# Kernel optimization log

Hardware: AMD Instinct MI355X
Metric: run time of the kernel (lower is better)

## Reference

```python
import jax, jax.numpy as jnp
import numpy as np

SEQ_LEN = 4096
HIDDEN = 1280
NUM_HEADS = 16
HEAD_DIM = HIDDEN // NUM_HEADS  # 80
NUM_SEQS = 8


def setup_inputs() -> dict:
    key = jax.random.key(0)
    ks = jax.random.split(key, 8)
    x = jax.random.normal(ks[0], (SEQ_LEN, HIDDEN), dtype=jnp.float32)
    # rotary tables: use cos/sin of random angles so they are bounded like real RoPE tables
    ang = jax.random.uniform(ks[1], (SEQ_LEN, HEAD_DIM), dtype=jnp.float32) * 6.283185
    cos = jnp.cos(ang)
    sin = jnp.sin(ang)
    # variable-length packed segments: strictly increasing boundaries incl. 0 and SEQ_LEN
    rng = np.random.default_rng(0)
    inner = np.sort(rng.choice(np.arange(1, SEQ_LEN), size=NUM_SEQS - 1, replace=False))
    cu_seqlens = jnp.asarray(np.concatenate([[0], inner, [SEQ_LEN]]), dtype=jnp.int32)
    s = 0.02
    w_qkv = jax.random.normal(ks[2], (HIDDEN, 3 * HIDDEN), dtype=jnp.float32) * s
    b_qkv = jnp.zeros((3 * HIDDEN,), dtype=jnp.float32)
    w_proj = jax.random.normal(ks[3], (HIDDEN, HIDDEN), dtype=jnp.float32) * s
    b_proj = jnp.zeros((HIDDEN,), dtype=jnp.float32)
    return {"x": x, "cu_seqlens": cu_seqlens, "cos": cos, "sin": sin,
            "w_qkv": w_qkv, "b_qkv": b_qkv, "w_proj": w_proj, "b_proj": b_proj}


def _rotate_half(t):
    d = t.shape[-1] // 2
    return jnp.concatenate([-t[..., d:], t[..., :d]], axis=-1)


def _apply_rope(q, k, cos, sin):
    # q,k: (S,H,D); cos,sin: (S,D) broadcast over heads, computed in fp32
    c = cos[:, None, :].astype(jnp.float32)
    s = sin[:, None, :].astype(jnp.float32)
    qf, kf = q.astype(jnp.float32), k.astype(jnp.float32)
    q_out = qf * c + _rotate_half(qf) * s
    k_out = kf * c + _rotate_half(kf) * s
    return q_out.astype(q.dtype), k_out.astype(k.dtype)


def reference(x, cu_seqlens, cos, sin, w_qkv, b_qkv, w_proj, b_proj):
    S = x.shape[0]
    scale = HEAD_DIM ** (-0.5)
    qkv = (x @ w_qkv + b_qkv).reshape(S, 3, NUM_HEADS, HEAD_DIM)
    q, k, v = qkv[:, 0], qkv[:, 1], qkv[:, 2]  # each (S,H,D)
    q, k = _apply_rope(q, k, cos, sin)
    # block-diagonal varlen attention via segment-id mask (same math as per-chunk softmax)
    pos = jnp.arange(S)
    seg = jnp.searchsorted(cu_seqlens[1:], pos, side='right')  # (S,) segment id
    mask = seg[:, None] == seg[None, :]  # (S,S) block-diagonal
    scores = jnp.einsum('shd,thd->hst', q, k) * scale  # (H,S,S)
    scores = jnp.where(mask[None], scores.astype(jnp.float32), jnp.finfo(jnp.float32).min)
    attn = jax.nn.softmax(scores, axis=-1).astype(q.dtype)
    out = jnp.einsum('hst,thd->shd', attn, v).reshape(S, NUM_HEADS * HEAD_DIM)
    return out @ w_proj + b_proj
```

## Files before the change

### kernel.cpp

```cpp
#include <hip/hip_runtime.h>
#include <cstdint>
#include <cstddef>

typedef __bf16 bf16x8 __attribute__((ext_vector_type(8)));
typedef float f32x4 __attribute__((ext_vector_type(4)));

#define SEQ   4096
#define HID   1280
#define NH    16
#define HD    80

__device__ __forceinline__ unsigned short f2bf(float f) {
  unsigned int u = __float_as_uint(f);
  unsigned int r = u + 0x7FFFu + ((u >> 16) & 1u);
  return (unsigned short)(r >> 16);
}
__device__ __forceinline__ float bf2f(unsigned short h) {
  return __uint_as_float(((unsigned int)h) << 16);
}
__device__ __forceinline__ __bf16 us2bf(unsigned short u) {
  union { unsigned short s; __bf16 b; } c; c.s = u; return c.b;
}
__device__ __forceinline__ void dma16(const void* g, void* l) {
  __builtin_amdgcn_global_load_lds((const __attribute__((address_space(1))) unsigned int*)g,
                                   (__attribute__((address_space(3))) unsigned int*)l, 16, 0, 0);
}

__global__ __launch_bounds__(256) void split_hi_kernel(const float* __restrict__ x,
                                                       unsigned short* __restrict__ hi,
                                                       int n4) {
  int i = blockIdx.x * 256 + threadIdx.x;
  if (i >= n4) return;
  float4 v = *((const float4*)x + i);
  *((ushort4*)hi + i) = make_ushort4(f2bf(v.x), f2bf(v.y), f2bf(v.z), f2bf(v.w));
}

__global__ __launch_bounds__(256) void tsplit_kernel(const float* __restrict__ W,
                                                     unsigned short* __restrict__ Thi,
                                                     unsigned short* __restrict__ Tlo,
                                                     int K, int N) {
  __shared__ float tile[32][33];
  int n0 = blockIdx.x * 32, k0 = blockIdx.y * 32;
  int tx = threadIdx.x & 31, ty = threadIdx.x >> 5;
#pragma unroll
  for (int i = 0; i < 32; i += 8)
    tile[ty + i][tx] = W[(size_t)(k0 + ty + i) * N + n0 + tx];
  __syncthreads();
#pragma unroll
  for (int i = 0; i < 32; i += 8) {
    float v = tile[tx][ty + i];
    size_t idx = (size_t)(n0 + ty + i) * K + (size_t)(k0 + tx);
    unsigned short h = f2bf(v);
    Thi[idx] = h;
    Tlo[idx] = f2bf(v - bf2f(h));
  }
}

__global__ __launch_bounds__(256, 3) void gemm128_x2(
    const unsigned short* __restrict__ A, const unsigned short* __restrict__ Bh,
    const unsigned short* __restrict__ Bl, const float* __restrict__ bias,
    float* __restrict__ out0, float* __restrict__ out1, float* __restrict__ out2,
    int M, int N, int K) {
  __shared__ __align__(16) unsigned short sALL[3 * 8192];

  const int t = threadIdx.x;
  const int lane = t & 63, wave = t >> 6;
  const int c16 = lane & 15, quad = lane >> 4;
  const int bm = blockIdx.y * 128, bn = blockIdx.x * 128;
  const int wr = (wave >> 1) * 64, wc = (wave & 1) * 64;
  const int lrow = lane >> 3;
  const int lswz = (lane & 7) ^ lrow;

  f32x4 acc[4][4];
#pragma unroll
  for (int i = 0; i < 4; ++i)
#pragma unroll
    for (int j = 0; j < 4; ++j) acc[i][j] = (f32x4){0.f, 0.f, 0.f, 0.f};

  const unsigned short* gp[12];
#pragma unroll
  for (int i = 0; i < 12; ++i) {
    const int ua = wave * 12 + i;
    const int arr = ua >> 4, sub = ua & 15;
    const unsigned short* g = (arr == 0) ? A : (arr == 1) ? Bh : Bl;
    const int rowg = ((arr == 0) ? bm : bn) + sub * 8 + lrow;
    gp[i] = g + (size_t)rowg * K + lswz * 8;
  }

  for (int k0 = 0; k0 < K; k0 += 64) {
    __syncthreads();
#pragma unroll
    for (int i = 0; i < 12; ++i)
      dma16(gp[i] + k0, &sALL[(wave * 12 + i) * 512]);
    __syncthreads();
#pragma unroll
    for (int ks = 0; ks < 2; ++ks) {
      bf16x8 a[4], bh[4], bl[4];
#pragma unroll
      for (int mi = 0; mi < 4; ++mi) {
        const int row = wr + mi * 16 + c16;
        const int off = row * 64 + (((ks * 4 + quad) ^ (row & 7)) * 8);
        a[mi] = *(const bf16x8*)&sALL[off];
      }
#pragma unroll
      for (int ni = 0; ni < 4; ++ni) {
        const int row = wc + ni * 16 + c16;
        const int off = row * 64 + (((ks * 4 + quad) ^ (row & 7)) * 8);
        bh[ni] = *(const bf16x8*)&sALL[8192 + off];
        bl[ni] = *(const bf16x8*)&sALL[16384 + off];
      }
#pragma unroll
      for (int mi = 0; mi < 4; ++mi)
#pragma unroll
        for (int ni = 0; ni < 4; ++ni) {
          acc[mi][ni] = __builtin_amdgcn_mfma_f32_16x16x32_bf16(a[mi], bh[ni], acc[mi][ni], 0, 0, 0);
          acc[mi][ni] = __builtin_amdgcn_mfma_f32_16x16x32_bf16(a[mi], bl[ni], acc[mi][ni], 0, 0, 0);
        }
    }
  }
#pragma unroll
  for (int ni = 0; ni < 4; ++ni) {
    int colg = bn + wc + ni * 16 + c16;
    float bv = bias[colg];
    float* op;
    int c = colg;
    if (c < 1280) op = out0;
    else if (c < 2560) { op = out1; c -= 1280; }
    else { op = out2; c -= 2560; }
#pragma unroll
    for (int mi = 0; mi < 4; ++mi)
#pragma unroll
      for (int r = 0; r < 4; ++r) {
        int rowg = bm + wr + mi * 16 + quad * 4 + r;
        op[(size_t)rowg * 1280 + c] = acc[mi][ni][r] + bv;
      }
  }
}

__global__ __launch_bounds__(256) void rope_pack_kernel(
    float* __restrict__ qf, const float* __restrict__ kf,
    const float* __restrict__ cs, const float* __restrict__ sn,
    unsigned short* __restrict__ khi, unsigned short* __restrict__ klo) {
  const int h = blockIdx.y;
  const int s = blockIdx.x * 64 + (threadIdx.x >> 2);
  const int p = threadIdx.x & 3;
  float* qrow = qf + (size_t)s * HID + h * HD;
  const float* krow = kf + (size_t)s * HID + h * HD;
  const float* cr = cs + (size_t)s * HD;
  const float* sr = sn + (size_t)s * HD;
  unsigned short* kh = khi + ((size_t)h * SEQ + s) * HD;
  unsigned short* kl = klo + ((size_t)h * SEQ + s) * HD;
#pragma unroll
  for (int j = 0; j < 10; ++j) {
    int d = 10 * p + j;
    float c0 = cr[d], s0 = sr[d], c1 = cr[d + 40], s1 = sr[d + 40];
    float q0 = qrow[d], q1 = qrow[d + 40];
    qrow[d]      = q0 * c0 - q1 * s0;
    qrow[d + 40] = q1 * c1 + q0 * s1;
    float k0 = krow[d], k1 = krow[d + 40];
    float kn0 = k0 * c0 - k1 * s0;
    float kn1 = k1 * c1 + k0 * s1;
    unsigned short h0 = f2bf(kn0), h1 = f2bf(kn1);
    kh[d] = h0;      kl[d] = f2bf(kn0 - bf2f(h0));
    kh[d + 40] = h1; kl[d + 40] = f2bf(kn1 - bf2f(h1));
  }
}

__global__ __launch_bounds__(256) void vt_pack_kernel(const float* __restrict__ vf,
                                                      unsigned short* __restrict__ vthi,
                                                      unsigned short* __restrict__ vtlo,
                                                      unsigned int* __restrict__ ctr) {
  if (blockIdx.x == 0 && blockIdx.y == 0 && threadIdx.x == 0) *ctr = 0u;
  __shared__ unsigned short sTh[80][72];
  __shared__ unsigned short sTl[80][72];
  const int h = blockIdx.y;
  const int s0 = blockIdx.x * 64;
  const int t = threadIdx.x;
  {
    int row = t >> 2, p = (t & 3) * 20;
    const float* src = vf + (size_t)(s0 + row) * HID + h * HD + p;
#pragma unroll
    for (int i = 0; i < 5; ++i) {
      float4 v = *(const float4*)(src + 4 * i);
      float vv[4] = {v.x, v.y, v.z, v.w};
#pragma unroll
      for (int j = 0; j < 4; ++j) {
        int d = p + 4 * i + j;
        unsigned short hu = f2bf(vv[j]);
        sTh[d][row] = hu;
        sTl[d][row] = f2bf(vv[j] - bf2f(hu));
      }
    }
  }
  __syncthreads();
  if (t < 160) {
    int d = t >> 1, half = (t & 1) * 32;
    size_t base = (size_t)(h * HD + d) * SEQ + s0 + half;
#pragma unroll
    for (int i = 0; i < 8; ++i) {
      *(ushort4*)&vthi[base + 4 * i] = *(ushort4*)&sTh[d][half + 4 * i];
      *(ushort4*)&vtlo[base + 4 * i] = *(ushort4*)&sTl[d][half + 4 * i];
    }
  }
}


#define SMAX(SC, MI, LI, PK, AR, KBLO, KBHI)                                   \
  do {                                                                         \
    float mx = -1e30f;                                                         \
    _Pragma("unroll") for (int nt = 0; nt < 4; ++nt)                           \
        _Pragma("unroll") for (int r = 0; r < 4; ++r) {                        \
      const int kg = ck + nt * 16 + quad * 4 + r;                              \
      const bool ok = (kg >= (KBLO)) && (kg < (KBHI));                         \
      float v = ok ? SC[nt][r] : -1e30f;                                       \
      SC[nt][r] = v;                                                           \
      mx = fmaxf(mx, v);                                                       \
    }                                                                          \
    mx = fmaxf(mx, __shfl_xor(mx, 16));                                        \
    mx = fmaxf(mx, __shfl_xor(mx, 32));                                        \
    const float mnew = fmaxf(MI, mx);                                          \
    const float alpha = __expf(MI - mnew);                                     \
    float ps = 0.f;                                                            \
    _Pragma("unroll") for (int nt = 0; nt < 4; ++nt)                           \
        _Pragma("unroll") for (int r = 0; r < 4; ++r) {                        \
      const float s = SC[nt][r];                                               \
      const float p = (s > -1e29f) ? __expf(s - mnew) : 0.f;                   \
      ps += p;                                                                 \
      const unsigned int pu = __float_as_uint(p);                              \
      const unsigned short ph_ = (unsigned short)(pu >> 16);                   \
      const unsigned short pl_ = f2bf(p - bf2f(ph_));                          \
      PK[nt][r] = (unsigned int)ph_ | ((unsigned int)pl_ << 16);               \
    }                                                                          \
    ps += __shfl_xor(ps, 16);                                                  \
    ps += __shfl_xor(ps, 32);                                                  \
    LI = LI * alpha + ps;                                                      \
    MI = mnew;                                                                 \
    _Pragma("unroll") for (int r = 0; r < 4; ++r)                              \
        AR[r] = __uint_as_float((unsigned)__builtin_amdgcn_ds_bpermute(        \
            (quad * 4 + r) << 2, __float_as_int(alpha)));                      \
  } while (0)

#define BUILD_P(PK, PHU, PLU)                                                  \
  do {                                                                         \
    unsigned int vj[8];                                                        \
    _Pragma("unroll") for (int j = 0; j < 8; ++j) {                            \
      const int addr = (j < 4) ? addrA : addrB;                                \
      const int r = j & 3;                                                     \
      const int v0 = __builtin_amdgcn_ds_bpermute(addr, (int)PK[2 * ks + 0][r]); \
      const int v1 = __builtin_amdgcn_ds_bpermute(addr, (int)PK[2 * ks + 1][r]); \
      vj[j] = (unsigned int)((quad & 2) ? v1 : v0);                            \
    }                                                                          \
    PHU.w[0] = __builtin_amdgcn_perm(vj[1], vj[0], 0x05040100u);               \
    PHU.w[1] = __builtin_amdgcn_perm(vj[3], vj[2], 0x05040100u);               \
    PHU.w[2] = __builtin_amdgcn_perm(vj[5], vj[4], 0x05040100u);               \
    PHU.w[3] = __builtin_amdgcn_perm(vj[7], vj[6], 0x05040100u);               \
    PLU.w[0] = __builtin_amdgcn_perm(vj[1], vj[0], 0x07060302u);               \
    PLU.w[1] = __builtin_amdgcn_perm(vj[3], vj[2], 0x07060302u);               \
    PLU.w[2] = __builtin_amdgcn_perm(vj[5], vj[4], 0x07060302u);               \
    PLU.w[3] = __builtin_amdgcn_perm(vj[7], vj[6], 0x07060302u);               \
  } while (0)

__global__ __launch_bounds__(256, 2) void attn_kernel(
    const float* __restrict__ qf, const unsigned short* __restrict__ khi,
    const unsigned short* __restrict__ klo, const unsigned short* __restrict__ vthi,
    const unsigned short* __restrict__ vtlo, const int* __restrict__ cu,
    unsigned short* __restrict__ ohi) {
  __shared__ __align__(16) unsigned short sKh[2][5120], sKl[2][5120];
  __shared__ __align__(16) unsigned short sVh[2][5120], sVl[2][5120];

  const int t = threadIdx.x;
  const int lane = t & 63, wave = t >> 6;
  const int c16 = lane & 15, quad = lane >> 4;
  const int lr8 = lane >> 3;
  const int vswz = (lane & 7) ^ lr8;
  const int addrA = ((((2 * quad) & 3) * 16) + c16) << 2;
  const int addrB = ((((2 * quad + 1) & 3) * 16) + c16) << 2;

  const unsigned int u = (blockIdx.x & 7) * 64 + (blockIdx.x >> 3);
  const int h = (int)(u >> 5);
  const int r0 = (int)(u & 31u) * 128;

  int cu_r[9];
#pragma unroll
  for (int i = 0; i < 9; ++i) cu_r[i] = cu[i];

  const int q0 = r0 + wave * 16 + c16;
  const int q1 = q0 + 64;
  int sq0 = 0, sq1 = 0, sg0 = 0, sg1 = 0;
#pragma unroll
  for (int i = 1; i < 8; ++i) {
    sq0 += (q0 >= cu_r[i]) ? 1 : 0;
    sq1 += (q1 >= cu_r[i]) ? 1 : 0;
    sg0 += (r0 >= cu_r[i]) ? 1 : 0;
    sg1 += (r0 + 127 >= cu_r[i]) ? 1 : 0;
  }
  const int kb_lo0 = cu_r[sq0], kb_hi0 = cu_r[sq0 + 1];
  const int kb_lo1 = cu_r[sq1], kb_hi1 = cu_r[sq1 + 1];
  const int ck0 = cu_r[sg0] & ~63;
  const int kend = cu_r[sg1 + 1];
  const int nchunk = (kend - ck0 + 63) >> 6;

  const float qsc = 0.11180339887498949f;
  bf16x8 qh0[3], ql0[3], qh1[3], ql1[3];
  {
    const float* qrowA = qf + (size_t)q0 * HID + h * HD;
    const float* qrowB = qf + (size_t)q1 * HID + h * HD;
#pragma unroll
    for (int ks = 0; ks < 3; ++ks) {
      const int d = ks * 32 + quad * 8;
      bf16x8 hA = {}, lA = {}, hB = {}, lB = {};
      if (d < 80) {
        float4 a0 = *(const float4*)(qrowA + d);
        float4 a1 = *(const float4*)(qrowA + d + 4);
        float4 b0 = *(const float4*)(qrowB + d);
        float4 b1 = *(const float4*)(qrowB + d + 4);
        float va[8] = {a0.x, a0.y, a0.z, a0.w, a1.x, a1.y, a1.z, a1.w};
        float vb[8] = {b0.x, b0.y, b0.z, b0.w, b1.x, b1.y, b1.z, b1.w};
#pragma unroll
        for (int j = 0; j < 8; ++j) {
          float v = va[j] * qsc;
          unsigned short hu = f2bf(v);
          hA[j] = us2bf(hu); lA[j] = us2bf(f2bf(v - bf2f(hu)));
          v = vb[j] * qsc;
          hu = f2bf(v);
          hB[j] = us2bf(hu); lB[j] = us2bf(f2bf(v - bf2f(hu)));
        }
      }
      qh0[ks] = hA; ql0[ks] = lA; qh1[ks] = hB; ql1[ks] = lB;
    }
  }

  f32x4 O0[5], O1[5];
#pragma unroll
  for (int dt = 0; dt < 5; ++dt) {
    O0[dt] = (f32x4){0.f, 0.f, 0.f, 0.f};
    O1[dt] = (f32x4){0.f, 0.f, 0.f, 0.f};
  }
  float m0 = -1e30f, l0v = 0.f, m1 = -1e30f, l1v = 0.f;

  auto STAGE = [&](int buf, int ck) {
    const unsigned short* gk = (wave & 2) ? klo : khi;
    unsigned short* lk = ((wave & 2) ? sKl[buf] : sKh[buf]) + (wave & 1) * 2560;
    const size_t kb = ((size_t)h * SEQ + ck) * 80 + (size_t)(wave & 1) * 2560 + lane * 8;
#pragma unroll
    for (int i2 = 0; i2 < 5; ++i2) dma16(gk + kb + i2 * 512, lk + i2 * 512);
    const unsigned short* gv = (wave & 2) ? vtlo : vthi;
    unsigned short* lv = (wave & 2) ? sVl[buf] : sVh[buf];
    const int half5 = (wave & 1) * 5;
#pragma unroll
    for (int i2 = 0; i2 < 5; ++i2) {
      const int uu = half5 + i2;
      dma16(gv + (size_t)(h * HD + 8 * uu + lr8) * SEQ + ck + vswz * 8, lv + uu * 512);
    }
  };

  STAGE(0, ck0);
  int cur = 0;

  for (int ci = 0; ci < nchunk; ++ci) {
    const int ck = ck0 + ci * 64;
    __syncthreads();
    if (ci + 1 < nchunk) STAGE(cur ^ 1, ck + 64);

    f32x4 sc0[4], sc1[4];
#pragma unroll
    for (int nt = 0; nt < 4; ++nt) {
      sc0[nt] = (f32x4){0.f, 0.f, 0.f, 0.f};
      sc1[nt] = (f32x4){0.f, 0.f, 0.f, 0.f};
    }
    __builtin_amdgcn_s_setprio(1);
#pragma unroll
    for (int nt = 0; nt < 4; ++nt) {
      const int krow = nt * 16 + c16;
#pragma unroll
      for (int ks = 0; ks < 3; ++ks) {
        const int d = ks * 32 + quad * 8;
        bf16x8 kh = {}, kl = {};
        if (d < 80) {
          kh = *(const bf16x8*)&sKh[cur][krow * 80 + d];
          kl = *(const bf16x8*)&sKl[cur][krow * 80 + d];
        }
        sc0[nt] = __builtin_amdgcn_mfma_f32_16x16x32_bf16(kh, qh0[ks], sc0[nt], 0, 0, 0);
        sc0[nt] = __builtin_amdgcn_mfma_f32_16x16x32_bf16(kh, ql0[ks], sc0[nt], 0, 0, 0);
        sc0[nt] = __builtin_amdgcn_mfma_f32_16x16x32_bf16(kl, qh0[ks], sc0[nt], 0, 0, 0);
        sc1[nt] = __builtin_amdgcn_mfma_f32_16x16x32_bf16(kh, qh1[ks], sc1[nt], 0, 0, 0);
        sc1[nt] = __builtin_amdgcn_mfma_f32_16x16x32_bf16(kh, ql1[ks], sc1[nt], 0, 0, 0);
        sc1[nt] = __builtin_amdgcn_mfma_f32_16x16x32_bf16(kl, qh1[ks], sc1[nt], 0, 0, 0);
      }
    }
    __builtin_amdgcn_s_setprio(0);

    unsigned int pk0[4][4], pk1[4][4];
    float aR0[4], aR1[4];
    SMAX(sc0, m0, l0v, pk0, aR0, kb_lo0, kb_hi0);
    SMAX(sc1, m1, l1v, pk1, aR1, kb_lo1, kb_hi1);
#pragma unroll
    for (int dt = 0; dt < 5; ++dt) {
      f32x4 o = O0[dt];
      o[0] *= aR0[0]; o[1] *= aR0[1]; o[2] *= aR0[2]; o[3] *= aR0[3];
      O0[dt] = o;
      o = O1[dt];
      o[0] *= aR1[0]; o[1] *= aR1[1]; o[2] *= aR1[2]; o[3] *= aR1[3];
      O1[dt] = o;
    }

#pragma unroll
    for (int ks = 0; ks < 2; ++ks) {
      union { unsigned int w[4]; bf16x8 v; } ph0u, pl0u, ph1u, pl1u;
      BUILD_P(pk0, ph0u, pl0u);
      BUILD_P(pk1, ph1u, pl1u);
      const int g = ks * 4 + quad;
      __builtin_amdgcn_s_setprio(1);
#pragma unroll
      for (int dt = 0; dt < 5; ++dt) {
        const int d = dt * 16 + c16;
        const int off = d * 64 + ((g ^ (d & 7)) * 8);
        bf16x8 vh = *(const bf16x8*)&sVh[cur][off];
        bf16x8 vl = *(const bf16x8*)&sVl[cur][off];
        O0[dt] = __builtin_amdgcn_mfma_f32_16x16x32_bf16(ph0u.v, vh, O0[dt], 0, 0, 0);
        O0[dt] = __builtin_amdgcn_mfma_f32_16x16x32_bf16(ph0u.v, vl, O0[dt], 0, 0, 0);
        O0[dt] = __builtin_amdgcn_mfma_f32_16x16x32_bf16(pl0u.v, vh, O0[dt], 0, 0, 0);
        O1[dt] = __builtin_amdgcn_mfma_f32_16x16x32_bf16(ph1u.v, vh, O1[dt], 0, 0, 0);
        O1[dt] = __builtin_amdgcn_mfma_f32_16x16x32_bf16(ph1u.v, vl, O1[dt], 0, 0, 0);
        O1[dt] = __builtin_amdgcn_mfma_f32_16x16x32_bf16(pl1u.v, vh, O1[dt], 0, 0, 0);
      }
      __builtin_amdgcn_s_setprio(0);
    }
    cur ^= 1;
  }

  const float inv0 = 1.0f / l0v;
  const float inv1 = 1.0f / l1v;
  float iR0[4], iR1[4];
#pragma unroll
  for (int r = 0; r < 4; ++r) {
    iR0[r] = __uint_as_float((unsigned)__builtin_amdgcn_ds_bpermute(
                 (quad * 4 + r) << 2, __float_as_int(inv0)));
    iR1[r] = __uint_as_float((unsigned)__builtin_amdgcn_ds_bpermute(
                 (quad * 4 + r) << 2, __float_as_int(inv1)));
  }
#pragma unroll
  for (int dt = 0; dt < 5; ++dt)
#pragma unroll
    for (int r = 0; r < 4; ++r) {
      const int row0 = r0 + wave * 16 + quad * 4 + r;
      ohi[(size_t)row0 * HID + h * HD + dt * 16 + c16] = f2bf(O0[dt][r] * iR0[r]);
      ohi[(size_t)(row0 + 64) * HID + h * HD + dt * 16 + c16] = f2bf(O1[dt][r] * iR1[r]);
    }
}

extern "C" void kernel_launch(void* const* d_in, const int* in_sizes, int n_in,
                              void* d_out, int out_size, void* d_ws, size_t ws_size,
                              hipStream_t stream) {
  const float* x      = (const float*)d_in[0];
  const int*   cu     = (const int*)d_in[1];
  const float* cs     = (const float*)d_in[2];
  const float* sn     = (const float*)d_in[3];
  const float* w_qkv  = (const float*)d_in[4];
  const float* b_qkv  = (const float*)d_in[5];
  const float* w_proj = (const float*)d_in[6];
  const float* b_proj = (const float*)d_in[7];
  float* out = (float*)d_out;

  char* ws = (char*)d_ws;
  float*          qf     = (float*)(ws + 0);
  float*          kf     = (float*)(ws + 20971520ULL);
  unsigned short* vthi   = (unsigned short*)(ws + 20971520ULL);
  unsigned short* vtlo   = (unsigned short*)(ws + 31457280ULL);
  float*          vf     = (float*)(ws + 41943040ULL);
  unsigned short* o_hi   = (unsigned short*)(ws + 41943040ULL);
  unsigned short* x_hi   = (unsigned short*)(ws + 62914560ULL);
  unsigned short* khi    = (unsigned short*)(ws + 62914560ULL);
  unsigned short* klo    = (unsigned short*)(ws + 73400320ULL);
  unsigned short* wqt_hi = (unsigned short*)(ws + 83886080ULL);
  unsigned short* wqt_lo = (unsigned short*)(ws + 93716480ULL);
  unsigned short* wpt_hi = (unsigned short*)(ws + 103546880ULL);
  unsigned short* wpt_lo = (unsigned short*)(ws + 106823680ULL);
  unsigned int*   ctr    = (unsigned int*)(ws + 83886080ULL);

  split_hi_kernel<<<5120, 256, 0, stream>>>(x, x_hi, 1310720);
  tsplit_kernel<<<dim3(120, 40), 256, 0, stream>>>(w_qkv, wqt_hi, wqt_lo, 1280, 3840);
  tsplit_kernel<<<dim3(40, 40), 256, 0, stream>>>(w_proj, wpt_hi, wpt_lo, 1280, 1280);
  gemm128_x2<<<dim3(30, 32), 256, 0, stream>>>(x_hi, wqt_hi, wqt_lo, b_qkv,
                                               qf, kf, vf, 4096, 3840, 1280);
  rope_pack_kernel<<<dim3(64, 16), 256, 0, stream>>>(qf, kf, cs, sn, khi, klo);
  vt_pack_kernel<<<dim3(64, 16), 256, 0, stream>>>(vf, vthi, vtlo, ctr);
  attn_kernel<<<512, 256, 0, stream>>>(qf, khi, klo, vthi, vtlo, cu, o_hi);
  gemm128_x2<<<dim3(10, 32), 256, 0, stream>>>(o_hi, wpt_hi, wpt_lo, b_proj,
                                               out, nullptr, nullptr, 4096, 1280, 1280);
}
```

Baseline: 410.4 us.

## Shrink attention blocks to 64 rows and split K/V staging into single buffers

The attention kernel now runs 1024 blocks of 128 threads, each covering 64 query rows instead of 128, which doubles grid parallelism and tightens the key range for each block. Shared memory drops from double-buffered to single-buffered K and V. Loads are staggered so the next K tile is fetched during the PV phase and the next V tile during the next QK phase. This adds extra barriers per chunk and re-reads K/V across more blocks. The unused counter reset in vt_pack is also removed.

```diff
diff --git a/kernel.cpp b/kernel.cpp
--- a/kernel.cpp
+++ b/kernel.cpp
@@ -168,9 +168,7 @@
 
 __global__ __launch_bounds__(256) void vt_pack_kernel(const float* __restrict__ vf,
                                                       unsigned short* __restrict__ vthi,
-                                                      unsigned short* __restrict__ vtlo,
-                                                      unsigned int* __restrict__ ctr) {
-  if (blockIdx.x == 0 && blockIdx.y == 0 && threadIdx.x == 0) *ctr = 0u;
+                                                      unsigned short* __restrict__ vtlo) {
   __shared__ unsigned short sTh[80][72];
   __shared__ unsigned short sTl[80][72];
   const int h = blockIdx.y;
@@ -260,13 +258,13 @@
     PLU.w[3] = __builtin_amdgcn_perm(vj[7], vj[6], 0x07060302u);               \
   } while (0)
 
-__global__ __launch_bounds__(256, 2) void attn_kernel(
+__global__ __launch_bounds__(128, 2) void attn_kernel(
     const float* __restrict__ qf, const unsigned short* __restrict__ khi,
     const unsigned short* __restrict__ klo, const unsigned short* __restrict__ vthi,
     const unsigned short* __restrict__ vtlo, const int* __restrict__ cu,
     unsigned short* __restrict__ ohi) {
-  __shared__ __align__(16) unsigned short sKh[2][5120], sKl[2][5120];
-  __shared__ __align__(16) unsigned short sVh[2][5120], sVl[2][5120];
+  __shared__ __align__(16) unsigned short sKh[5120], sKl[5120];
+  __shared__ __align__(16) unsigned short sVh[5120], sVl[5120];
 
   const int t = threadIdx.x;
   const int lane = t & 63, wave = t >> 6;
@@ -276,23 +274,23 @@
   const int addrA = ((((2 * quad) & 3) * 16) + c16) << 2;
   const int addrB = ((((2 * quad + 1) & 3) * 16) + c16) << 2;
 
-  const unsigned int u = (blockIdx.x & 7) * 64 + (blockIdx.x >> 3);
-  const int h = (int)(u >> 5);
-  const int r0 = (int)(u & 31u) * 128;
+  const unsigned int u = (blockIdx.x & 7) * 128 + (blockIdx.x >> 3);
+  const int h = (int)(u >> 6);
+  const int r0 = (int)(u & 63u) * 64;
 
   int cu_r[9];
 #pragma unroll
   for (int i = 0; i < 9; ++i) cu_r[i] = cu[i];
 
   const int q0 = r0 + wave * 16 + c16;
-  const int q1 = q0 + 64;
+  const int q1 = q0 + 32;
   int sq0 = 0, sq1 = 0, sg0 = 0, sg1 = 0;
 #pragma unroll
   for (int i = 1; i < 8; ++i) {
     sq0 += (q0 >= cu_r[i]) ? 1 : 0;
     sq1 += (q1 >= cu_r[i]) ? 1 : 0;
     sg0 += (r0 >= cu_r[i]) ? 1 : 0;
-    sg1 += (r0 + 127 >= cu_r[i]) ? 1 : 0;
+    sg1 += (r0 + 63 >= cu_r[i]) ? 1 : 0;
   }
   const int kb_lo0 = cu_r[sq0], kb_hi0 = cu_r[sq0 + 1];
   const int kb_lo1 = cu_r[sq1], kb_hi1 = cu_r[sq1 + 1];
@@ -338,29 +336,27 @@
   }
   float m0 = -1e30f, l0v = 0.f, m1 = -1e30f, l1v = 0.f;
 
-  auto STAGE = [&](int buf, int ck) {
-    const unsigned short* gk = (wave & 2) ? klo : khi;
-    unsigned short* lk = ((wave & 2) ? sKl[buf] : sKh[buf]) + (wave & 1) * 2560;
-    const size_t kb = ((size_t)h * SEQ + ck) * 80 + (size_t)(wave & 1) * 2560 + lane * 8;
-#pragma unroll
-    for (int i2 = 0; i2 < 5; ++i2) dma16(gk + kb + i2 * 512, lk + i2 * 512);
-    const unsigned short* gv = (wave & 2) ? vtlo : vthi;
-    unsigned short* lv = (wave & 2) ? sVl[buf] : sVh[buf];
-    const int half5 = (wave & 1) * 5;
-#pragma unroll
-    for (int i2 = 0; i2 < 5; ++i2) {
-      const int uu = half5 + i2;
-      dma16(gv + (size_t)(h * HD + 8 * uu + lr8) * SEQ + ck + vswz * 8, lv + uu * 512);
-    }
+  auto STAGE_K = [&](int ck) {
+    const unsigned short* gk = (wave & 1) ? klo : khi;
+    unsigned short* lk = (wave & 1) ? sKl : sKh;
+    const size_t kb = ((size_t)h * SEQ + ck) * 80 + lane * 8;
+#pragma unroll
+    for (int i2 = 0; i2 < 10; ++i2) dma16(gk + kb + i2 * 512, lk + i2 * 512);
   };
-
-  STAGE(0, ck0);
-  int cur = 0;
+  auto STAGE_V = [&](int ck) {
+    const unsigned short* gv = (wave & 1) ? vtlo : vthi;
+    unsigned short* lv = (wave & 1) ? sVl : sVh;
+#pragma unroll
+    for (int i2 = 0; i2 < 10; ++i2)
+      dma16(gv + (size_t)(h * HD + 8 * i2 + lr8) * SEQ + ck + vswz * 8, lv + i2 * 512);
+  };
+
+  STAGE_K(ck0);
+  STAGE_V(ck0);
+  __syncthreads();
 
   for (int ci = 0; ci < nchunk; ++ci) {
     const int ck = ck0 + ci * 64;
-    __syncthreads();
-    if (ci + 1 < nchunk) STAGE(cur ^ 1, ck + 64);
 
     f32x4 sc0[4], sc1[4];
 #pragma unroll
@@ -377,8 +373,8 @@
         const int d = ks * 32 + quad * 8;
         bf16x8 kh = {}, kl = {};
         if (d < 80) {
-          kh = *(const bf16x8*)&sKh[cur][krow * 80 + d];
-          kl = *(const bf16x8*)&sKl[cur][krow * 80 + d];
+          kh = *(const bf16x8*)&sKh[krow * 80 + d];
+          kl = *(const bf16x8*)&sKl[krow * 80 + d];
         }
         sc0[nt] = __builtin_amdgcn_mfma_f32_16x16x32_bf16(kh, qh0[ks], sc0[nt], 0, 0, 0);
         sc0[nt] = __builtin_amdgcn_mfma_f32_16x16x32_bf16(kh, ql0[ks], sc0[nt], 0, 0, 0);
@@ -404,6 +400,9 @@
       O1[dt] = o;
     }
 
+    __syncthreads();
+    if (ci + 1 < nchunk) STAGE_K(ck + 64);
+
 #pragma unroll
     for (int ks = 0; ks < 2; ++ks) {
       union { unsigned int w[4]; bf16x8 v; } ph0u, pl0u, ph1u, pl1u;
@@ -415,8 +414,8 @@
       for (int dt = 0; dt < 5; ++dt) {
         const int d = dt * 16 + c16;
         const int off = d * 64 + ((g ^ (d & 7)) * 8);
-        bf16x8 vh = *(const bf16x8*)&sVh[cur][off];
-        bf16x8 vl = *(const bf16x8*)&sVl[cur][off];
+        bf16x8 vh = *(const bf16x8*)&sVh[off];
+        bf16x8 vl = *(const bf16x8*)&sVl[off];
         O0[dt] = __builtin_amdgcn_mfma_f32_16x16x32_bf16(ph0u.v, vh, O0[dt], 0, 0, 0);
         O0[dt] = __builtin_amdgcn_mfma_f32_16x16x32_bf16(ph0u.v, vl, O0[dt], 0, 0, 0);
         O0[dt] = __builtin_amdgcn_mfma_f32_16x16x32_bf16(pl0u.v, vh, O0[dt], 0, 0, 0);
@@ -426,7 +425,9 @@
       }
       __builtin_amdgcn_s_setprio(0);
     }
-    cur ^= 1;
+
+    __syncthreads();
+    if (ci + 1 < nchunk) STAGE_V(ck + 64);
   }
 
   const float inv0 = 1.0f / l0v;
@@ -445,7 +446,7 @@
     for (int r = 0; r < 4; ++r) {
       const int row0 = r0 + wave * 16 + quad * 4 + r;
       ohi[(size_t)row0 * HID + h * HD + dt * 16 + c16] = f2bf(O0[dt][r] * iR0[r]);
-      ohi[(size_t)(row0 + 64) * HID + h * HD + dt * 16 + c16] = f2bf(O1[dt][r] * iR1[r]);
+      ohi[(size_t)(row0 + 32) * HID + h * HD + dt * 16 + c16] = f2bf(O1[dt][r] * iR1[r]);
     }
 }
 
@@ -476,7 +477,6 @@
   unsigned short* wqt_lo = (unsigned short*)(ws + 93716480ULL);
   unsigned short* wpt_hi = (unsigned short*)(ws + 103546880ULL);
   unsigned short* wpt_lo = (unsigned short*)(ws + 106823680ULL);
-  unsigned int*   ctr    = (unsigned int*)(ws + 83886080ULL);
 
   split_hi_kernel<<<5120, 256, 0, stream>>>(x, x_hi, 1310720);
   tsplit_kernel<<<dim3(120, 40), 256, 0, stream>>>(w_qkv, wqt_hi, wqt_lo, 1280, 3840);
@@ -484,8 +484,8 @@
   gemm128_x2<<<dim3(30, 32), 256, 0, stream>>>(x_hi, wqt_hi, wqt_lo, b_qkv,
                                                qf, kf, vf, 4096, 3840, 1280);
   rope_pack_kernel<<<dim3(64, 16), 256, 0, stream>>>(qf, kf, cs, sn, khi, klo);
-  vt_pack_kernel<<<dim3(64, 16), 256, 0, stream>>>(vf, vthi, vtlo, ctr);
-  attn_kernel<<<512, 256, 0, stream>>>(qf, khi, klo, vthi, vtlo, cu, o_hi);
+  vt_pack_kernel<<<dim3(64, 16), 256, 0, stream>>>(vf, vthi, vtlo);
+  attn_kernel<<<1024, 128, 0, stream>>>(qf, khi, klo, vthi, vtlo, cu, o_hi);
   gemm128_x2<<<dim3(10, 32), 256, 0, stream>>>(o_hi, wpt_hi, wpt_lo, b_proj,
                                                out, nullptr, nullptr, 4096, 1280, 1280);
 }
```

New measurement: 410.2 us. No clear change (-0.0%).
